# Optimization experiments

Hardware: AMD Instinct MI355X
Metric: run time of the kernel (lower is better)

## Reference

```python
import jax, jax.numpy as jnp
import numpy as np

D_MODEL = 1024
N_HEADS = 16
D_K = D_MODEL // N_HEADS


def setup_inputs() -> dict:
    key = jax.random.key(0)
    ks = jax.random.split(key, 9)
    s = 1.0 / np.sqrt(D_MODEL)
    inp = {
        "x": jax.random.normal(ks[0], (2, 2048, D_MODEL), dtype=jnp.float32),
        "wq": jax.random.uniform(ks[1], (D_MODEL, D_MODEL), jnp.float32, -s, s),
        "bq": jax.random.uniform(ks[2], (D_MODEL,), jnp.float32, -s, s),
        "wk": jax.random.uniform(ks[3], (D_MODEL, D_MODEL), jnp.float32, -s, s),
        "bk": jax.random.uniform(ks[4], (D_MODEL,), jnp.float32, -s, s),
        "wv": jax.random.uniform(ks[5], (D_MODEL, D_MODEL), jnp.float32, -s, s),
        "bv": jax.random.uniform(ks[6], (D_MODEL,), jnp.float32, -s, s),
        "wo": jax.random.uniform(ks[7], (D_MODEL, D_MODEL), jnp.float32, -s, s),
        "bo": jax.random.uniform(ks[8], (D_MODEL,), jnp.float32, -s, s),
    }
    return inp


def reference(x, wq, bq, wk, bk, wv, bv, wo, bo):
    B, S, _ = x.shape
    # projections; weights stored as [in, out] (torch Linear applies x @ W^T; here W pre-transposed)
    def proj(w, b):
        y = x @ w + b  # [B,S,D]
        return y.reshape(B, S, N_HEADS, D_K).transpose(0, 2, 1, 3)  # [B,H,S,dk]
    q, k, v = proj(wq, bq), proj(wk, bk), proj(wv, bv)
    scores = jnp.einsum('bhqd,bhkd->bhqk', q, k) / jnp.sqrt(jnp.float32(D_K))
    attn = jax.nn.softmax(scores, axis=-1)  # dropout p=0 -> identity
    ctx = jnp.einsum('bhqk,bhkd->bhqd', attn, v)
    ctx = ctx.transpose(0, 2, 1, 3).reshape(B, S, D_MODEL)
    return ctx @ wo + bo
```

## Files before the change

kernel.cpp:

```cpp
#include <hip/hip_runtime.h>
#include <hip/hip_bf16.h>
#include <math.h>


typedef __attribute__((ext_vector_type(8))) short bf8v;
typedef __attribute__((ext_vector_type(4))) float f32x4;
typedef __attribute__((ext_vector_type(16))) float f32x16;

#define mfma32(a, b, c) __builtin_amdgcn_mfma_f32_32x32x16_bf16((a), (b), (c), 0, 0, 0)

constexpr int Dm = 1024;
constexpr int NH = 16;
constexpr int DK = 64;
constexpr int BB = 2;
constexpr int SS = 2048;
constexpr int MM = BB * SS;

__device__ __forceinline__ unsigned short f2bf(float f) {
  union { float f; unsigned u; } v; v.f = f;
  unsigned r = v.u + 0x7fffu + ((v.u >> 16) & 1u);
  return (unsigned short)(r >> 16);
}

__device__ __forceinline__ unsigned cvt_pk_bf16(float lo, float hi) {
  unsigned r;
  asm("v_cvt_pk_bf16_f32 %0, %1, %2" : "=v"(r) : "v"(lo), "v"(hi));
  return r;
}

__device__ __forceinline__ void swap32(unsigned &a, unsigned &b) {
  asm("v_permlane32_swap_b32 %0, %1" : "+v"(a), "+v"(b));
}

__device__ __forceinline__ void gl_lds16(const void* g, void* l) {
  __builtin_amdgcn_global_load_lds(
      (const __attribute__((address_space(1))) void*)g,
      (__attribute__((address_space(3))) void*)l, 16, 0, 0);
}

__device__ __forceinline__ int swz4(int r) { return (r ^ (r >> 2)) & 3; }
__device__ __forceinline__ bf8v frag4(const unsigned short* base, int R, int s0) {
  return *(const bf8v*)((const char*)base + R * 64 + ((s0 ^ swz4(R)) << 4));
}
__device__ __forceinline__ bf8v rd8(const unsigned short* base, int row, int slot) {
  return *(const bf8v*)((const char*)base + row * 128 + (((slot ^ row) & 7) << 4));
}

__global__ __launch_bounds__(256) void transw_kernel(
    const float* __restrict__ w0, const float* __restrict__ w1,
    const float* __restrict__ w2, const float* __restrict__ w3,
    unsigned short* __restrict__ dstBase)
{
  const float* src = (blockIdx.y == 0) ? w0 : (blockIdx.y == 1) ? w1
                   : (blockIdx.y == 2) ? w2 : w3;
  unsigned short* dst = dstBase + (size_t)blockIdx.y * (Dm * Dm);
  int idx = blockIdx.x * 256 + threadIdx.x;
  int i = idx & (Dm - 1);
  int o = (idx >> 10) << 2;
  float4 v = *(const float4*)(src + (size_t)i * Dm + o);
  dst[(size_t)(o + 0) * Dm + i] = f2bf(v.x);
  dst[(size_t)(o + 1) * Dm + i] = f2bf(v.y);
  dst[(size_t)(o + 2) * Dm + i] = f2bf(v.z);
  dst[(size_t)(o + 3) * Dm + i] = f2bf(v.w);
}

__global__ __launch_bounds__(256) void xconv_kernel(
    const float* __restrict__ x, unsigned short* __restrict__ xb)
{
  int idx = blockIdx.x * 256 + threadIdx.x;
  const float* s = x + (size_t)idx * 8;
  float4 a = *(const float4*)s;
  float4 b = *(const float4*)(s + 4);
  union { bf8v v; unsigned w[4]; } u;
  u.w[0] = cvt_pk_bf16(a.x, a.y); u.w[1] = cvt_pk_bf16(a.z, a.w);
  u.w[2] = cvt_pk_bf16(b.x, b.y); u.w[3] = cvt_pk_bf16(b.z, b.w);
  *(bf8v*)(xb + (size_t)idx * 8) = u.v;
}

__global__ __launch_bounds__(256) void proj_kernel(
    const unsigned short* __restrict__ Xb, const unsigned short* __restrict__ WtBase,
    const float* __restrict__ bq, const float* __restrict__ bk, const float* __restrict__ bv,
    unsigned short* __restrict__ Qh, unsigned short* __restrict__ Kh,
    unsigned short* __restrict__ Vh)
{
  __shared__ unsigned short As[2][128 * 32];
  __shared__ unsigned short Bs[2][128 * 32];
  const int z = blockIdx.z;
  const unsigned short* W = WtBase + (size_t)z * (Dm * Dm);
  const float* bias = (z == 0) ? bq : (z == 1) ? bk : bv;

  const int tid = threadIdx.x, lane = tid & 63, wave = tid >> 6;
  const int wm = wave >> 1, wn = wave & 1;
  const int m0 = blockIdx.y * 128, n0 = blockIdx.x * 128;
  const int l15 = lane & 15, l4 = lane >> 4;

  const int q1 = tid, q2 = tid + 256;
  const int rw1 = q1 >> 2, sl1 = q1 & 3, c1 = sl1 ^ swz4(rw1);
  const int rw2 = q2 >> 2, sl2 = q2 & 3, c2 = sl2 ^ swz4(rw2);
  const int ldsOff1 = (q1 - lane) * 16, ldsOff2 = (q2 - lane) * 16;

  auto stageAB = [&](int buf, int k0) {
    gl_lds16(Xb + (size_t)(m0 + rw1) * Dm + k0 + c1 * 8, (char*)As[buf] + ldsOff1);
    gl_lds16(Xb + (size_t)(m0 + rw2) * Dm + k0 + c2 * 8, (char*)As[buf] + ldsOff2);
    gl_lds16(W + (size_t)(n0 + rw1) * Dm + k0 + c1 * 8, (char*)Bs[buf] + ldsOff1);
    gl_lds16(W + (size_t)(n0 + rw2) * Dm + k0 + c2 * 8, (char*)Bs[buf] + ldsOff2);
  };

  f32x4 acc[4][4] = {};

  stageAB(0, 0);
  __syncthreads();

  for (int k0 = 0; k0 < Dm; k0 += 32) {
    const int cur = (k0 >> 5) & 1, nxt = cur ^ 1;
    if (k0 + 32 < Dm) stageAB(nxt, k0 + 32);

    bf8v af[4], bfr[4];
    #pragma unroll
    for (int i = 0; i < 4; ++i) af[i] = frag4(As[cur], wm * 64 + i * 16 + l15, l4);
    #pragma unroll
    for (int j = 0; j < 4; ++j) bfr[j] = frag4(Bs[cur], wn * 64 + j * 16 + l15, l4);
    __builtin_amdgcn_s_setprio(1);
    #pragma unroll
    for (int i = 0; i < 4; ++i)
      #pragma unroll
      for (int j = 0; j < 4; ++j)
        acc[i][j] = __builtin_amdgcn_mfma_f32_16x16x32_bf16(af[i], bfr[j], acc[i][j], 0, 0, 0);
    __builtin_amdgcn_s_setprio(0);
    __syncthreads();
  }

  unsigned short* Out = (z == 0) ? Qh : (z == 1) ? Kh : Vh;
  const float oscale = (z == 0) ? 0.18033688011112042f : 1.0f;
  #pragma unroll
  for (int i = 0; i < 4; ++i)
    #pragma unroll
    for (int j = 0; j < 4; ++j) {
      int row = m0 + wm * 64 + i * 16 + l4 * 4;
      int col = n0 + wn * 64 + j * 16 + l15;
      float bcol = bias[col];
      int h = col >> 6, d = col & 63;
      #pragma unroll
      for (int r = 0; r < 4; ++r) {
        int rr = row + r;
        int b = rr >> 11, s = rr & 2047;
        unsigned short val = f2bf((acc[i][j][r] + bcol) * oscale);
        if (z < 2)
          Out[(((size_t)(b * NH + h) * SS + s) * DK) + d] = val;
        else
          Out[((size_t)(b * NH + h) * DK + d) * SS + s] = val;
      }
    }
}

__global__ __launch_bounds__(256) void outproj_kernel(
    const unsigned short* __restrict__ Ctx, const unsigned short* __restrict__ Wto,
    const float* __restrict__ bo, float* __restrict__ Out)
{
  __shared__ unsigned short As[2][128 * 32];
  __shared__ unsigned short Bs[2][128 * 32];
  const int tid = threadIdx.x, lane = tid & 63, wave = tid >> 6;
  const int wm = wave >> 1, wn = wave & 1;
  const int m0 = blockIdx.y * 128, n0 = blockIdx.x * 128;
  const int l15 = lane & 15, l4 = lane >> 4;

  const int q1 = tid, q2 = tid + 256;
  const int rw1 = q1 >> 2, sl1 = q1 & 3, c1 = sl1 ^ swz4(rw1);
  const int rw2 = q2 >> 2, sl2 = q2 & 3, c2 = sl2 ^ swz4(rw2);
  const int ldsOff1 = (q1 - lane) * 16, ldsOff2 = (q2 - lane) * 16;

  auto srcA = [&](int rw, int c, int k0) -> const unsigned short* {
    int rr = m0 + rw, b = rr >> 11, s = rr & 2047;
    int col = k0 + c * 8, h = col >> 6, d = col & 63;
    return Ctx + ((size_t)(b * NH + h) * SS + s) * DK + d;
  };
  auto stageAB = [&](int buf, int k0) {
    gl_lds16(srcA(rw1, c1, k0), (char*)As[buf] + ldsOff1);
    gl_lds16(srcA(rw2, c2, k0), (char*)As[buf] + ldsOff2);
    gl_lds16(Wto + (size_t)(n0 + rw1) * Dm + k0 + c1 * 8, (char*)Bs[buf] + ldsOff1);
    gl_lds16(Wto + (size_t)(n0 + rw2) * Dm + k0 + c2 * 8, (char*)Bs[buf] + ldsOff2);
  };

  f32x4 acc[4][4] = {};

  stageAB(0, 0);
  __syncthreads();

  for (int k0 = 0; k0 < Dm; k0 += 32) {
    const int cur = (k0 >> 5) & 1, nxt = cur ^ 1;
    if (k0 + 32 < Dm) stageAB(nxt, k0 + 32);

    bf8v af[4], bfr[4];
    #pragma unroll
    for (int i = 0; i < 4; ++i) af[i] = frag4(As[cur], wm * 64 + i * 16 + l15, l4);
    #pragma unroll
    for (int j = 0; j < 4; ++j) bfr[j] = frag4(Bs[cur], wn * 64 + j * 16 + l15, l4);
    __builtin_amdgcn_s_setprio(1);
    #pragma unroll
    for (int i = 0; i < 4; ++i)
      #pragma unroll
      for (int j = 0; j < 4; ++j)
        acc[i][j] = __builtin_amdgcn_mfma_f32_16x16x32_bf16(af[i], bfr[j], acc[i][j], 0, 0, 0);
    __builtin_amdgcn_s_setprio(0);
    __syncthreads();
  }

  #pragma unroll
  for (int i = 0; i < 4; ++i)
    #pragma unroll
    for (int j = 0; j < 4; ++j) {
      int row = m0 + wm * 64 + i * 16 + l4 * 4;
      int col = n0 + wn * 64 + j * 16 + l15;
      float bcol = bo[col];
      #pragma unroll
      for (int r = 0; r < 4; ++r)
        Out[(size_t)(row + r) * Dm + col] = acc[i][j][r] + bcol;
    }
}

__global__ __launch_bounds__(512, 4) void attn_kernel(
    const unsigned short* __restrict__ Q, const unsigned short* __restrict__ K,
    const unsigned short* __restrict__ Vt, unsigned short* __restrict__ CtxQ)
{
  __shared__ __align__(16) unsigned short smem[32768];
  unsigned short* KlB = smem;
  unsigned short* VlB = smem + 16384;

  const int tid = threadIdx.x, lane = tid & 63, wave = tid >> 6;
  const int qsub = wave & 3, khalf = wave >> 2;
  const int l31 = lane & 31, hi = lane >> 5;
  const int bh = blockIdx.y;
  const int q0 = blockIdx.x * 128 + qsub * 32;
  const size_t base = (size_t)bh * SS * DK;

  bf8v qf[4];
  #pragma unroll
  for (int dc = 0; dc < 4; ++dc)
    qf[dc] = *(const bf8v*)(Q + base + (size_t)(q0 + l31) * DK + dc * 16 + hi * 8);

  bf8v onesv;
  #pragma unroll
  for (int e = 0; e < 8; ++e) onesv[e] = (short)0x3F80;

  f32x16 cacc[2] = {};
  f32x16 lacc = {};

  const int srow = tid >> 3, ssl = tid & 7, sc = ssl ^ (srow & 7);
  const int soff = (tid - lane) * 16;
  auto kslab = [&](int buf, int h) { return KlB + (buf * 2 + h) * 4096; };
  auto vslab = [&](int buf, int h) { return VlB + (buf * 2 + h) * 4096; };
  auto stage = [&](int buf, int kt) {
    gl_lds16(K + base + (size_t)(kt + srow) * DK + sc * 8,          (char*)kslab(buf, 0) + soff);
    gl_lds16(K + base + (size_t)(1024 + kt + srow) * DK + sc * 8,   (char*)kslab(buf, 1) + soff);
    gl_lds16(Vt + base + (size_t)srow * SS + kt + sc * 8,           (char*)vslab(buf, 0) + soff);
    gl_lds16(Vt + base + (size_t)srow * SS + 1024 + kt + sc * 8,    (char*)vslab(buf, 1) + soff);
  };

  constexpr int NT = 16;
  stage(0, 0);
  __syncthreads();

  for (int t = 0; t < NT; ++t) {
    const int cur = t & 1;
    if (t + 1 < NT) stage(cur ^ 1, (t + 1) * 64);
    const unsigned short* Kb = kslab(cur, khalf);
    const unsigned short* Vb = vslab(cur, khalf);

    f32x16 st0 = {}, st1 = {};
    __builtin_amdgcn_s_setprio(1);
    #pragma unroll
    for (int dc = 0; dc < 4; ++dc) {
      bf8v kf0 = rd8(Kb, l31, dc * 2 + hi);
      bf8v kf1 = rd8(Kb, 32 + l31, dc * 2 + hi);
      st0 = mfma32(kf0, qf[dc], st0);
      st1 = mfma32(kf1, qf[dc], st1);
    }
    __builtin_amdgcn_s_setprio(0);

    auto process = [&](const f32x16& st, int ktile) {
      float p[16];
      #pragma unroll
      for (int r = 0; r < 16; ++r) p[r] = exp2f(st[r]);
      #pragma unroll
      for (int c = 0; c < 2; ++c) {
        const int o = c * 8;
        unsigned A  = cvt_pk_bf16(p[o + 0], p[o + 1]);
        unsigned B  = cvt_pk_bf16(p[o + 4], p[o + 5]);
        unsigned Cw = cvt_pk_bf16(p[o + 2], p[o + 3]);
        unsigned Dw = cvt_pk_bf16(p[o + 6], p[o + 7]);
        swap32(A, B); swap32(Cw, Dw);
        union { bf8v v; unsigned w[4]; } pf;
        pf.w[0] = A; pf.w[1] = Cw; pf.w[2] = B; pf.w[3] = Dw;
        const int slot = ktile * 4 + c * 2 + hi;
        bf8v vb0 = rd8(Vb, l31, slot);
        bf8v vb1 = rd8(Vb, 32 + l31, slot);
        __builtin_amdgcn_s_setprio(1);
        cacc[0] = mfma32(vb0, pf.v, cacc[0]);
        cacc[1] = mfma32(vb1, pf.v, cacc[1]);
        lacc    = mfma32(onesv, pf.v, lacc);
        __builtin_amdgcn_s_setprio(0);
      }
    };
    process(st0, 0);
    process(st1, 1);

    __syncthreads();
  }

  float lf = lacc[0];
  float* scr = (float*)smem;
  float* fs = scr + qsub * 2112;

  if (khalf == 1) {
    #pragma unroll
    for (int n = 0; n < 2; ++n)
      #pragma unroll
      for (int r = 0; r < 16; ++r)
        fs[(n * 16 + r) * 64 + lane] = cacc[n][r];
    fs[2048 + lane] = lf;
  }
  __syncthreads();
  if (khalf == 0) {
    float inv = 1.0f / (lf + fs[2048 + lane]);
    #pragma unroll
    for (int n = 0; n < 2; ++n)
      #pragma unroll
      for (int j = 0; j < 4; ++j) {
        float v0 = (cacc[n][4 * j + 0] + fs[(n * 16 + 4 * j + 0) * 64 + lane]) * inv;
        float v1 = (cacc[n][4 * j + 1] + fs[(n * 16 + 4 * j + 1) * 64 + lane]) * inv;
        float v2 = (cacc[n][4 * j + 2] + fs[(n * 16 + 4 * j + 2) * 64 + lane]) * inv;
        float v3 = (cacc[n][4 * j + 3] + fs[(n * 16 + 4 * j + 3) * 64 + lane]) * inv;
        uint2 w;
        w.x = cvt_pk_bf16(v0, v1);
        w.y = cvt_pk_bf16(v2, v3);
        int d = n * 32 + 8 * j + 4 * hi;
        *(uint2*)(CtxQ + base + (size_t)(q0 + l31) * DK + d) = w;
      }
  }
}

extern "C" void kernel_launch(void* const* d_in, const int* in_sizes, int n_in,
                              void* d_out, int out_size, void* d_ws, size_t ws_size,
                              hipStream_t stream) {
  const float* x  = (const float*)d_in[0];
  const float* wq = (const float*)d_in[1];
  const float* bq = (const float*)d_in[2];
  const float* wk = (const float*)d_in[3];
  const float* bk = (const float*)d_in[4];
  const float* wv = (const float*)d_in[5];
  const float* bv = (const float*)d_in[6];
  const float* wo = (const float*)d_in[7];
  const float* bo = (const float*)d_in[8];
  float* out = (float*)d_out;

  unsigned short* ws = (unsigned short*)d_ws;
  const size_t WPLANE = (size_t)Dm * Dm;
  const size_t PLANE  = (size_t)MM * Dm;
  unsigned short* Wt  = ws;
  unsigned short* Qh  = ws + PLANE;
  unsigned short* Kh  = ws + 2 * PLANE;
  unsigned short* Vh  = ws + 3 * PLANE;
  unsigned short* Wto = Wt + 3 * WPLANE;
  unsigned short* Xb  = (unsigned short*)d_out;

  transw_kernel<<<dim3(1024, 4), dim3(256), 0, stream>>>(wq, wk, wv, wo, Wt);
  xconv_kernel<<<dim3(2048), dim3(256), 0, stream>>>(x, Xb);
  proj_kernel<<<dim3(Dm / 128, MM / 128, 3), dim3(256), 0, stream>>>(
      Xb, Wt, bq, bk, bv, Qh, Kh, Vh);
  attn_kernel<<<dim3(SS / 128, BB * NH), dim3(512), 0, stream>>>(Qh, Kh, Vh, Qh);
  outproj_kernel<<<dim3(Dm / 128, MM / 128), dim3(256), 0, stream>>>(Qh, Wto, bo, out);
}
```

Before: 133.8 us.

## Restructure attention into 64-query tiles with four-way key split and direct V loads

The attention kernel now handles 64 queries per block (2 query subgroups × 4 key splits) instead of 128, launched as a flat 1024-block grid whose block index is remapped to spread heads across the grid. K is staged through LDS in 128-key tiles, while V fragments are read directly from global memory rather than staged. The row sum is computed with scalar adds instead of an extra ones-vector MFMA, and the four key-split partials are merged in a two-step LDS tree reduction. This aims to raise occupancy and parallelism and drop the extra MFMA, at the cost of uncached global V reads and extra reduction syncs.

```diff
diff --git a/kernel.cpp b/kernel.cpp
--- a/kernel.cpp
+++ b/kernel.cpp
@@ -222,15 +222,16 @@
     const unsigned short* __restrict__ Q, const unsigned short* __restrict__ K,
     const unsigned short* __restrict__ Vt, unsigned short* __restrict__ CtxQ)
 {
-  __shared__ __align__(16) unsigned short smem[32768];
-  unsigned short* KlB = smem;
-  unsigned short* VlB = smem + 16384;
+  __shared__ __align__(16) unsigned short smem[17408];
 
   const int tid = threadIdx.x, lane = tid & 63, wave = tid >> 6;
-  const int qsub = wave & 3, khalf = wave >> 2;
+  const int qsub = wave & 1, ks = wave >> 1;
   const int l31 = lane & 31, hi = lane >> 5;
-  const int bh = blockIdx.y;
-  const int q0 = blockIdx.x * 128 + qsub * 32;
+
+  const int fid = blockIdx.x;
+  const int bh = ((fid & 7) << 2) | ((fid >> 3) & 3);
+  const int qtile = fid >> 5;
+  const int q0 = qtile * 64 + qsub * 32;
   const size_t base = (size_t)bh * SS * DK;
 
   bf8v qf[4];
@@ -238,80 +239,71 @@
   for (int dc = 0; dc < 4; ++dc)
     qf[dc] = *(const bf8v*)(Q + base + (size_t)(q0 + l31) * DK + dc * 16 + hi * 8);
 
-  bf8v onesv;
-  #pragma unroll
-  for (int e = 0; e < 8; ++e) onesv[e] = (short)0x3F80;
-
   f32x16 cacc[2] = {};
-  f32x16 lacc = {};
-
-  const int srow = tid >> 3, ssl = tid & 7, sc = ssl ^ (srow & 7);
-  const int soff = (tid - lane) * 16;
-  auto kslab = [&](int buf, int h) { return KlB + (buf * 2 + h) * 4096; };
-  auto vslab = [&](int buf, int h) { return VlB + (buf * 2 + h) * 4096; };
+  float lsum = 0.f;
+
+  const int c1q = tid, c2q = tid + 512;
+  const int rwa = c1q >> 3, sla = c1q & 7, ca = sla ^ (rwa & 7);
+  const int rwb = c2q >> 3, slb = c2q & 7, cb = slb ^ (rwb & 7);
+  const int offa = (c1q - lane) * 16, offb = (c2q - lane) * 16;
+  auto kslab = [&](int buf) { return smem + buf * 8192; };
   auto stage = [&](int buf, int kt) {
-    gl_lds16(K + base + (size_t)(kt + srow) * DK + sc * 8,          (char*)kslab(buf, 0) + soff);
-    gl_lds16(K + base + (size_t)(1024 + kt + srow) * DK + sc * 8,   (char*)kslab(buf, 1) + soff);
-    gl_lds16(Vt + base + (size_t)srow * SS + kt + sc * 8,           (char*)vslab(buf, 0) + soff);
-    gl_lds16(Vt + base + (size_t)srow * SS + 1024 + kt + sc * 8,    (char*)vslab(buf, 1) + soff);
+    gl_lds16(K + base + (size_t)(kt + rwa) * DK + ca * 8, (char*)kslab(buf) + offa);
+    gl_lds16(K + base + (size_t)(kt + rwb) * DK + cb * 8, (char*)kslab(buf) + offb);
   };
 
-  constexpr int NT = 16;
+  constexpr int NT = SS / 128;
   stage(0, 0);
   __syncthreads();
 
   for (int t = 0; t < NT; ++t) {
     const int cur = t & 1;
-    if (t + 1 < NT) stage(cur ^ 1, (t + 1) * 64);
-    const unsigned short* Kb = kslab(cur, khalf);
-    const unsigned short* Vb = vslab(cur, khalf);
-
-    f32x16 st0 = {}, st1 = {};
+    if (t + 1 < NT) stage(cur ^ 1, (t + 1) * 128);
+    const unsigned short* Kb = kslab(cur);
+    const int keybase = t * 128 + ks * 32;
+
+    f32x16 st = {};
     __builtin_amdgcn_s_setprio(1);
     #pragma unroll
     for (int dc = 0; dc < 4; ++dc) {
-      bf8v kf0 = rd8(Kb, l31, dc * 2 + hi);
-      bf8v kf1 = rd8(Kb, 32 + l31, dc * 2 + hi);
-      st0 = mfma32(kf0, qf[dc], st0);
-      st1 = mfma32(kf1, qf[dc], st1);
+      bf8v kf = rd8(Kb, ks * 32 + l31, dc * 2 + hi);
+      st = mfma32(kf, qf[dc], st);
     }
     __builtin_amdgcn_s_setprio(0);
 
-    auto process = [&](const f32x16& st, int ktile) {
-      float p[16];
-      #pragma unroll
-      for (int r = 0; r < 16; ++r) p[r] = exp2f(st[r]);
-      #pragma unroll
-      for (int c = 0; c < 2; ++c) {
-        const int o = c * 8;
-        unsigned A  = cvt_pk_bf16(p[o + 0], p[o + 1]);
-        unsigned B  = cvt_pk_bf16(p[o + 4], p[o + 5]);
-        unsigned Cw = cvt_pk_bf16(p[o + 2], p[o + 3]);
-        unsigned Dw = cvt_pk_bf16(p[o + 6], p[o + 7]);
-        swap32(A, B); swap32(Cw, Dw);
-        union { bf8v v; unsigned w[4]; } pf;
-        pf.w[0] = A; pf.w[1] = Cw; pf.w[2] = B; pf.w[3] = Dw;
-        const int slot = ktile * 4 + c * 2 + hi;
-        bf8v vb0 = rd8(Vb, l31, slot);
-        bf8v vb1 = rd8(Vb, 32 + l31, slot);
-        __builtin_amdgcn_s_setprio(1);
-        cacc[0] = mfma32(vb0, pf.v, cacc[0]);
-        cacc[1] = mfma32(vb1, pf.v, cacc[1]);
-        lacc    = mfma32(onesv, pf.v, lacc);
-        __builtin_amdgcn_s_setprio(0);
-      }
-    };
-    process(st0, 0);
-    process(st1, 1);
+    float p[16];
+    #pragma unroll
+    for (int r = 0; r < 16; ++r) p[r] = exp2f(st[r]);
+    lsum += (((p[0] + p[1]) + (p[2] + p[3])) + ((p[4] + p[5]) + (p[6] + p[7])))
+          + (((p[8] + p[9]) + (p[10] + p[11])) + ((p[12] + p[13]) + (p[14] + p[15])));
+    #pragma unroll
+    for (int c = 0; c < 2; ++c) {
+      const int o = c * 8;
+      unsigned A  = cvt_pk_bf16(p[o + 0], p[o + 1]);
+      unsigned B  = cvt_pk_bf16(p[o + 4], p[o + 5]);
+      unsigned Cw = cvt_pk_bf16(p[o + 2], p[o + 3]);
+      unsigned Dw = cvt_pk_bf16(p[o + 6], p[o + 7]);
+      swap32(A, B); swap32(Cw, Dw);
+      union { bf8v v; unsigned w[4]; } pf;
+      pf.w[0] = A; pf.w[1] = Cw; pf.w[2] = B; pf.w[3] = Dw;
+      const int kv = keybase + (c * 2 + hi) * 8;
+      bf8v vb0 = *(const bf8v*)(Vt + base + (size_t)l31 * SS + kv);
+      bf8v vb1 = *(const bf8v*)(Vt + base + (size_t)(32 + l31) * SS + kv);
+      __builtin_amdgcn_s_setprio(1);
+      cacc[0] = mfma32(vb0, pf.v, cacc[0]);
+      cacc[1] = mfma32(vb1, pf.v, cacc[1]);
+      __builtin_amdgcn_s_setprio(0);
+    }
 
     __syncthreads();
   }
 
-  float lf = lacc[0];
+  float lf = lsum + __shfl_xor(lsum, 32);
   float* scr = (float*)smem;
-  float* fs = scr + qsub * 2112;
-
-  if (khalf == 1) {
+  float* rg[2] = { scr + qsub * 2112, scr + (2 + qsub) * 2112 };
+
+  if (ks == 1 || ks == 3) {
+    float* fs = rg[ks >> 1];
     #pragma unroll
     for (int n = 0; n < 2; ++n)
       #pragma unroll
@@ -320,7 +312,28 @@
     fs[2048 + lane] = lf;
   }
   __syncthreads();
-  if (khalf == 0) {
+  if (ks == 0 || ks == 2) {
+    float* fs = rg[ks >> 1];
+    #pragma unroll
+    for (int n = 0; n < 2; ++n)
+      #pragma unroll
+      for (int r = 0; r < 16; ++r)
+        cacc[n][r] += fs[(n * 16 + r) * 64 + lane];
+    lf += fs[2048 + lane];
+  }
+  __syncthreads();
+  if (ks == 2) {
+    float* fs = rg[0];
+    #pragma unroll
+    for (int n = 0; n < 2; ++n)
+      #pragma unroll
+      for (int r = 0; r < 16; ++r)
+        fs[(n * 16 + r) * 64 + lane] = cacc[n][r];
+    fs[2048 + lane] = lf;
+  }
+  __syncthreads();
+  if (ks == 0) {
+    float* fs = rg[0];
     float inv = 1.0f / (lf + fs[2048 + lane]);
     #pragma unroll
     for (int n = 0; n < 2; ++n)
@@ -367,6 +380,6 @@
   xconv_kernel<<<dim3(2048), dim3(256), 0, stream>>>(x, Xb);
   proj_kernel<<<dim3(Dm / 128, MM / 128, 3), dim3(256), 0, stream>>>(
       Xb, Wt, bq, bk, bv, Qh, Kh, Vh);
-  attn_kernel<<<dim3(SS / 128, BB * NH), dim3(512), 0, stream>>>(Qh, Kh, Vh, Qh);
+  attn_kernel<<<dim3(1024), dim3(512), 0, stream>>>(Qh, Kh, Vh, Qh);
   outproj_kernel<<<dim3(Dm / 128, MM / 128), dim3(256), 0, stream>>>(Qh, Wto, bo, out);
 }
```

Result: slower. 155.1 us (+15.9%).
